# Optimization experiments

Measured on AMD Instinct MI355X. Metric: run time of the kernel, lower is better.

Reference implementation:

```python
import jax, jax.numpy as jnp
import numpy as np

DIM = 96
HEADS = 6
WIN = (4, 4, 4)
SHIFT = (2, 2, 2)
MLP_HIDDEN = 384
GRID = (16, 64, 64)
B = 2
EPS = 1e-5


def _rel_idx():
    # relative position index [N, N] into the (2w-1)^3 bias table
    c = np.stack(np.meshgrid(*[np.arange(w) for w in WIN], indexing='ij')).reshape(3, -1)
    rel = c[:, :, None] - c[:, None, :]
    for d, w in enumerate(WIN):
        rel[d] += w - 1
    rel[0] *= (2 * WIN[1] - 1) * (2 * WIN[2] - 1)
    rel[1] *= 2 * WIN[2] - 1
    return jnp.asarray(rel.sum(0))

REL_IDX = _rel_idx()  # [64, 64]


def _layernorm(x, g, b):
    m = jnp.mean(x, axis=-1, keepdims=True)
    v = jnp.mean(jnp.square(x - m), axis=-1, keepdims=True)
    return (x - m) * jax.lax.rsqrt(v + EPS) * g + b


def setup_inputs() -> dict:
    key = jax.random.key(0)
    ks = jax.random.split(key, 8)
    nI, nX, nT = GRID
    L = nI * nX * nT
    std = 0.02
    return {
        'x': jax.random.normal(ks[0], (B, L, DIM), dtype=jnp.float32),
        'norm1_g': jnp.ones((DIM,), jnp.float32),
        'norm1_b': jnp.zeros((DIM,), jnp.float32),
        'qkv_w': jax.random.normal(ks[1], (DIM, 3 * DIM), jnp.float32) * std,
        'qkv_b': jnp.zeros((3 * DIM,), jnp.float32),
        'proj_w': jax.random.normal(ks[2], (DIM, DIM), jnp.float32) * std,
        'proj_b': jnp.zeros((DIM,), jnp.float32),
        'bias_table': jax.random.normal(ks[3], ((2 * WIN[0] - 1) * (2 * WIN[1] - 1) * (2 * WIN[2] - 1), HEADS), jnp.float32) * std,
        'norm2_g': jnp.ones((DIM,), jnp.float32),
        'norm2_b': jnp.zeros((DIM,), jnp.float32),
        'mlp_w1': jax.random.normal(ks[4], (DIM, MLP_HIDDEN), jnp.float32) * std,
        'mlp_b1': jnp.zeros((MLP_HIDDEN,), jnp.float32),
        'mlp_w2': jax.random.normal(ks[5], (MLP_HIDDEN, DIM), jnp.float32) * std,
        'mlp_b2': jnp.zeros((DIM,), jnp.float32),
        'nI': nI, 'nX': nX, 'nT': nT,
    }


def reference(x, norm1_g, norm1_b, qkv_w, qkv_b, proj_w, proj_b, bias_table,
              norm2_g, norm2_b, mlp_w1, mlp_b1, mlp_w2, mlp_b2, nI, nX, nT):
    Bb, L, C = x.shape
    wI, wX, wT = WIN
    sI, sX, sT = SHIFT
    N = wI * wX * wT
    hd = C // HEADS

    h = _layernorm(x, norm1_g, norm1_b).reshape(Bb, nI, nX, nT, C)
    h = jnp.roll(h, (-sI, -sX, -sT), axis=(1, 2, 3))
    # window partition -> [B*nW, N, C]
    h = h.reshape(Bb, nI // wI, wI, nX // wX, wX, nT // wT, wT, C)
    h = h.transpose(0, 1, 3, 5, 2, 4, 6, 7).reshape(-1, N, C)
    B_ = h.shape[0]

    qkv = (h @ qkv_w + qkv_b).reshape(B_, N, 3, HEADS, hd).transpose(2, 0, 3, 1, 4)
    q, k, v = qkv[0], qkv[1], qkv[2]  # each [B_, H, N, hd]
    attn = jnp.einsum('bhnd,bhmd->bhnm', q, k) * (hd ** -0.5)
    bias = bias_table[REL_IDX].transpose(2, 0, 1)  # [H, N, N]
    attn = jax.nn.softmax(attn + bias, axis=-1)
    o = jnp.einsum('bhnm,bhmd->bhnd', attn, v).transpose(0, 2, 1, 3).reshape(B_, N, C)
    o = o @ proj_w + proj_b

    # window reverse -> [B, nI, nX, nT, C]
    o = o.reshape(Bb, nI // wI, nX // wX, nT // wT, wI, wX, wT, C)
    o = o.transpose(0, 1, 4, 2, 5, 3, 6, 7).reshape(Bb, nI, nX, nT, C)
    o = jnp.roll(o, (sI, sX, sT), axis=(1, 2, 3)).reshape(Bb, L, C)

    x = x + o
    h2 = _layernorm(x, norm2_g, norm2_b)
    x = x + (jax.nn.gelu(h2 @ mlp_w1 + mlp_b1, approximate=False) @ mlp_w2 + mlp_b2)
    return x
```

## Files before the change

### kernel.cpp

```cpp
#include <hip/hip_runtime.h>
#include <math.h>


typedef __attribute__((ext_vector_type(8))) short short8;
typedef __attribute__((ext_vector_type(4))) float floatx4;
typedef unsigned short ushort;
typedef unsigned int uint;

__device__ __forceinline__ ushort f2bf(float f) {
    union { float f; uint u; } v; v.f = f;
    uint r = v.u + 0x7FFFu + ((v.u >> 16) & 1u);
    return (ushort)(r >> 16);
}
__device__ __forceinline__ uint pk2(float a, float b) {
    return (uint)f2bf(a) | ((uint)f2bf(b) << 16);
}
union U8 { uint u[4]; short8 s8; };

#define WS_QKV  0
#define WS_PROJ (288 * 104)
#define WS_W1   (384 * 104)
#define WS_W2   (768 * 104)

__global__ __launch_bounds__(512, 8)
void convert_w(const float* __restrict__ qkvw, const float* __restrict__ projw,
               const float* __restrict__ w1, const float* __restrict__ w2,
               ushort* __restrict__ ws)
{
    const int idx = blockIdx.x * 512 + threadIdx.x;
    const int kk = idx / 1152;
    const int r  = idx - kk * 1152;
    const int k0 = 2 * kk, k1 = k0 + 1;
    float a, b;
    if (r < 288)      { a = qkvw[k0 * 288 + r];              b = qkvw[k1 * 288 + r]; }
    else if (r < 384) { const int c = r - 288;  a = projw[k0 * 96 + c];  b = projw[k1 * 96 + c]; }
    else if (r < 768) { const int c = r - 384;  a = w1[k0 * 384 + c];    b = w1[k1 * 384 + c]; }
    else {
        const int c0 = r - 768;
        const int jt = c0 / 96, c = c0 - jt * 96;
        a = w2[(jt * 96 + k0) * 96 + c];
        b = w2[(jt * 96 + k1) * 96 + c];
    }
    *(uint*)&ws[r * 104 + k0] = pk2(a, b);
}

__global__ __launch_bounds__(512, 4)
void swin_attn_kernel(const float* __restrict__ x,
                      const float* __restrict__ n1g, const float* __restrict__ n1b,
                      const ushort* __restrict__ ws,
                      const float* __restrict__ qkvb,
                      const float* __restrict__ projb,
                      const float* __restrict__ btab,
                      float* __restrict__ y)
{
    __shared__ __align__(16) ushort hA[64 * 104];
    __shared__ __align__(16) ushort qS[6 * 64 * 20];
    __shared__ __align__(16) ushort kS[6 * 64 * 20];
    __shared__ __align__(16) ushort vT[6 * 16 * 68];
    __shared__ __align__(16) ushort oA[64 * 104];
    __shared__ __align__(16) float  bias_s[343 * 6];

    const int tid = threadIdx.x;
    const int wid = blockIdx.x;
    const int bb = wid >> 10;
    const int wi = (wid >> 8) & 3;
    const int wx = (wid >> 4) & 15;
    const int wt = wid & 15;

    for (int i = tid; i < 343 * 6; i += 512) bias_s[i] = btab[i];
    {
        const int n = tid >> 3, p = tid & 7;
        const int a = n >> 4, c = (n >> 2) & 3, e = n & 3;
        const int gi = (wi * 4 + a + 2) & 15;
        const int gx = (wx * 4 + c + 2) & 63;
        const int gt = (wt * 4 + e + 2) & 63;
        const int l = (gi << 12) + (gx << 6) + gt;
        const float* src = x + ((size_t)bb * 65536 + l) * 96 + p * 12;
        float v[12];
        #pragma unroll
        for (int i = 0; i < 3; ++i) {
            const float4 t = *(const float4*)(src + i * 4);
            v[i*4+0] = t.x; v[i*4+1] = t.y; v[i*4+2] = t.z; v[i*4+3] = t.w;
        }
        float s = 0.f, ss = 0.f;
        #pragma unroll
        for (int i = 0; i < 12; ++i) { s += v[i]; ss += v[i] * v[i]; }
        s  += __shfl_xor(s, 1);  s  += __shfl_xor(s, 2);  s  += __shfl_xor(s, 4);
        ss += __shfl_xor(ss, 1); ss += __shfl_xor(ss, 2); ss += __shfl_xor(ss, 4);
        const float mean = s * (1.f / 96.f);
        const float rstd = rsqrtf(ss * (1.f / 96.f) - mean * mean + 1e-5f);
        float nv[12];
        #pragma unroll
        for (int i = 0; i < 12; ++i) {
            const int ch = p * 12 + i;
            nv[i] = (v[i] - mean) * rstd * n1g[ch] + n1b[ch];
        }
        #pragma unroll
        for (int j = 0; j < 6; ++j)
            *(uint*)&hA[n * 104 + p * 12 + 2 * j] = pk2(nv[2*j], nv[2*j+1]);
    }
    __syncthreads();

    const int wv = tid >> 6, lane = tid & 63;
    const int lr = lane & 15, lg = lane >> 4;
    const int tr = wv >> 1;
    const int chf = wv & 1;

    const short8 hfr0 = *(const short8*)&hA[(tr*16 + lr) * 104 +  0 + lg * 8];
    const short8 hfr1 = *(const short8*)&hA[(tr*16 + lr) * 104 + 32 + lg * 8];
    const short8 hfr2 = *(const short8*)&hA[(tr*16 + lr) * 104 + 64 + lg * 8];

    #pragma unroll
    for (int jt = 0; jt < 3; ++jt) {
#define QKV_CT(CT) { \
        const ushort* wp = ws + WS_QKV + ((jt*96 + chf*48 + (CT)*16 + lr) * 104 + lg * 8); \
        floatx4 acc = {0.f,0.f,0.f,0.f}; \
        acc = __builtin_amdgcn_mfma_f32_16x16x32_bf16(*(const short8*)(wp     ), hfr0, acc, 0,0,0); \
        acc = __builtin_amdgcn_mfma_f32_16x16x32_bf16(*(const short8*)(wp + 32), hfr1, acc, 0,0,0); \
        acc = __builtin_amdgcn_mfma_f32_16x16x32_bf16(*(const short8*)(wp + 64), hfr2, acc, 0,0,0); \
        const int colb = chf*48 + (CT)*16 + lg*4; \
        const int hh = colb >> 4, db = colb & 15; \
        const int tok = tr*16 + lr; \
        const float4 b4 = *(const float4*)&qkvb[jt*96 + colb]; \
        const float v0 = acc[0] + b4.x, v1 = acc[1] + b4.y; \
        const float v2 = acc[2] + b4.z, v3 = acc[3] + b4.w; \
        if (jt == 0) { \
            *(uint*)&qS[(hh*64 + tok)*20 + db    ] = pk2(v0*0.25f, v1*0.25f); \
            *(uint*)&qS[(hh*64 + tok)*20 + db + 2] = pk2(v2*0.25f, v3*0.25f); \
        } else if (jt == 1) { \
            *(uint*)&kS[(hh*64 + tok)*20 + db    ] = pk2(v0, v1); \
            *(uint*)&kS[(hh*64 + tok)*20 + db + 2] = pk2(v2, v3); \
        } else { \
            vT[(hh*16 + db + 0)*68 + tok] = f2bf(v0); \
            vT[(hh*16 + db + 1)*68 + tok] = f2bf(v1); \
            vT[(hh*16 + db + 2)*68 + tok] = f2bf(v2); \
            vT[(hh*16 + db + 3)*68 + tok] = f2bf(v3); \
        } }
        QKV_CT(0) QKV_CT(1) QKV_CT(2)
#undef QKV_CT
    }
    __syncthreads();

    {
        const int c1 = lr >> 2, e1 = lr & 3;
        #pragma unroll
        for (int iu = 0; iu < 3; ++iu) {
            const int unit = wv * 3 + iu;
            const int head = unit >> 2, qt = unit & 3;
            U8 qf;
            { const uint2 qb = *(const uint2*)&qS[(head*64 + qt*16 + lr)*20 + lg*4];
              qf.u[0] = qb.x; qf.u[1] = qb.y; qf.u[2] = 0u; qf.u[3] = 0u; }
            float sc[16];
            #pragma unroll
            for (int kt = 0; kt < 4; ++kt) {
                U8 kf;
                { const uint2 kb = *(const uint2*)&kS[(head*64 + kt*16 + lr)*20 + lg*4];
                  kf.u[0] = kb.x; kf.u[1] = kb.y; kf.u[2] = 0u; kf.u[3] = 0u; }
                floatx4 z = {0.f,0.f,0.f,0.f};
                z = __builtin_amdgcn_mfma_f32_16x16x32_bf16(kf.s8, qf.s8, z, 0,0,0);
                #pragma unroll
                for (int r = 0; r < 4; ++r) {
                    const int ridx = ((qt - kt + 3)*7 + (c1 - lg + 3))*7 + (e1 - r + 3);
                    sc[kt*4+r] = z[r] + bias_s[ridx*6 + head];
                }
            }
            float mx = sc[0];
            #pragma unroll
            for (int j = 1; j < 16; ++j) mx = fmaxf(mx, sc[j]);
            float pn[16]; float sum = 0.f;
            #pragma unroll
            for (int j = 0; j < 16; ++j) { pn[j] = __expf(sc[j] - mx); sum += pn[j]; }
            const float inv = 1.f / sum;
            #pragma unroll
            for (int j = 0; j < 16; ++j) pn[j] *= inv;
            U8 pf0, pf1;
            pf0.u[0] = pk2(pn[0],  pn[1]);  pf0.u[1] = pk2(pn[2],  pn[3]);
            pf0.u[2] = pk2(pn[4],  pn[5]);  pf0.u[3] = pk2(pn[6],  pn[7]);
            pf1.u[0] = pk2(pn[8],  pn[9]);  pf1.u[1] = pk2(pn[10], pn[11]);
            pf1.u[2] = pk2(pn[12], pn[13]); pf1.u[3] = pk2(pn[14], pn[15]);
            U8 vf0, vf1;
            { const uint2 va = *(const uint2*)&vT[(head*16 + lr)*68 +  0 + lg*4];
              const uint2 vb = *(const uint2*)&vT[(head*16 + lr)*68 + 16 + lg*4];
              vf0.u[0] = va.x; vf0.u[1] = va.y; vf0.u[2] = vb.x; vf0.u[3] = vb.y; }
            { const uint2 va = *(const uint2*)&vT[(head*16 + lr)*68 + 32 + lg*4];
              const uint2 vb = *(const uint2*)&vT[(head*16 + lr)*68 + 48 + lg*4];
              vf1.u[0] = va.x; vf1.u[1] = va.y; vf1.u[2] = vb.x; vf1.u[3] = vb.y; }
            floatx4 o = {0.f,0.f,0.f,0.f};
            o = __builtin_amdgcn_mfma_f32_16x16x32_bf16(vf0.s8, pf0.s8, o, 0,0,0);
            o = __builtin_amdgcn_mfma_f32_16x16x32_bf16(vf1.s8, pf1.s8, o, 0,0,0);
            *(uint*)&oA[(qt*16 + lr)*104 + head*16 + lg*4    ] = pk2(o[0], o[1]);
            *(uint*)&oA[(qt*16 + lr)*104 + head*16 + lg*4 + 2] = pk2(o[2], o[3]);
        }
    }
    __syncthreads();

    {
        const short8 ofr0 = *(const short8*)&oA[(tr*16 + lr) * 104 +  0 + lg * 8];
        const short8 ofr1 = *(const short8*)&oA[(tr*16 + lr) * 104 + 32 + lg * 8];
        const short8 ofr2 = *(const short8*)&oA[(tr*16 + lr) * 104 + 64 + lg * 8];
        const int n = tr*16 + lr;
        const int gi = (wi * 4 + tr + 2) & 15;
        const int gx = (wx * 4 + (lr >> 2) + 2) & 63;
        const int gt = (wt * 4 + (lr & 3) + 2) & 63;
        const int l = (gi << 12) + (gx << 6) + gt;
        const size_t tbase = ((size_t)bb * 65536 + l) * 96;
        (void)n;
#define PRJ_CT(CT) { \
        const ushort* wp = ws + WS_PROJ + ((chf*48 + (CT)*16 + lr) * 104 + lg * 8); \
        floatx4 acc = {0.f,0.f,0.f,0.f}; \
        acc = __builtin_amdgcn_mfma_f32_16x16x32_bf16(*(const short8*)(wp     ), ofr0, acc, 0,0,0); \
        acc = __builtin_amdgcn_mfma_f32_16x16x32_bf16(*(const short8*)(wp + 32), ofr1, acc, 0,0,0); \
        acc = __builtin_amdgcn_mfma_f32_16x16x32_bf16(*(const short8*)(wp + 64), ofr2, acc, 0,0,0); \
        const int colb = chf*48 + (CT)*16 + lg*4; \
        const float4 pb4 = *(const float4*)&projb[colb]; \
        const float4 xv = *(const float4*)(x + tbase + colb); \
        float4 r; \
        r.x = xv.x + acc[0] + pb4.x; \
        r.y = xv.y + acc[1] + pb4.y; \
        r.z = xv.z + acc[2] + pb4.z; \
        r.w = xv.w + acc[3] + pb4.w; \
        *(float4*)(y + tbase + colb) = r; }
        PRJ_CT(0) PRJ_CT(1) PRJ_CT(2)
#undef PRJ_CT
    }
}

__global__ __launch_bounds__(512, 4)
void swin_mlp_kernel(const float* __restrict__ y,
                     const float* __restrict__ n2g, const float* __restrict__ n2b,
                     const ushort* __restrict__ ws,
                     const float* __restrict__ b1p, const float* __restrict__ b2p,
                     float* __restrict__ out)
{
    __shared__ __align__(16) ushort h2A[128 * 104];
    __shared__ __align__(16) ushort t1A[128 * 104];

    const int tid = threadIdx.x;
    const size_t tok0 = (size_t)blockIdx.x * 128;

    {
        const int tk = tid >> 2, q4 = tid & 3;
        const float* src = y + (tok0 + tk) * 96 + q4 * 24;
        float v[24];
        #pragma unroll
        for (int i = 0; i < 6; ++i) {
            const float4 t = *(const float4*)(src + i * 4);
            v[i*4+0]=t.x; v[i*4+1]=t.y; v[i*4+2]=t.z; v[i*4+3]=t.w;
        }
        float s = 0.f, ss = 0.f;
        #pragma unroll
        for (int i = 0; i < 24; ++i) { s += v[i]; ss += v[i]*v[i]; }
        s += __shfl_xor(s, 1); s += __shfl_xor(s, 2);
        ss += __shfl_xor(ss, 1); ss += __shfl_xor(ss, 2);
        const float mean = s * (1.f/96.f);
        const float rstd = rsqrtf(ss * (1.f/96.f) - mean*mean + 1e-5f);
        float nv[24];
        #pragma unroll
        for (int i = 0; i < 24; ++i) {
            const int ch = q4 * 24 + i;
            nv[i] = (v[i]-mean)*rstd*n2g[ch] + n2b[ch];
        }
        #pragma unroll
        for (int j = 0; j < 12; ++j)
            *(uint*)&h2A[tk * 104 + q4 * 24 + 2 * j] = pk2(nv[2*j], nv[2*j+1]);
    }
    __syncthreads();

    const int wv = tid >> 6, lane = tid & 63;
    const int lr = lane & 15, lg = lane >> 4;
    const int trow = (wv*16 + lr) * 104;

    const short8 hfr0 = *(const short8*)&h2A[trow +  0 + lg * 8];
    const short8 hfr1 = *(const short8*)&h2A[trow + 32 + lg * 8];
    const short8 hfr2 = *(const short8*)&h2A[trow + 64 + lg * 8];

    floatx4 a0 = {0.f,0.f,0.f,0.f}, a1 = {0.f,0.f,0.f,0.f}, a2 = {0.f,0.f,0.f,0.f},
            a3 = {0.f,0.f,0.f,0.f}, a4 = {0.f,0.f,0.f,0.f}, a5 = {0.f,0.f,0.f,0.f};

    #pragma unroll
    for (int jt = 0; jt < 4; ++jt) {
#define M1_CT(CT) { \
        const ushort* wp = ws + WS_W1 + ((jt*96 + (CT)*16 + lr) * 104 + lg * 8); \
        floatx4 g = {0.f,0.f,0.f,0.f}; \
        g = __builtin_amdgcn_mfma_f32_16x16x32_bf16(*(const short8*)(wp     ), hfr0, g, 0,0,0); \
        g = __builtin_amdgcn_mfma_f32_16x16x32_bf16(*(const short8*)(wp + 32), hfr1, g, 0,0,0); \
        g = __builtin_amdgcn_mfma_f32_16x16x32_bf16(*(const short8*)(wp + 64), hfr2, g, 0,0,0); \
        const float4 bv = *(const float4*)&b1p[jt*96 + (CT)*16 + lg*4]; \
        float t0 = g[0] + bv.x, t1 = g[1] + bv.y, t2 = g[2] + bv.z, t3 = g[3] + bv.w; \
        t0 = 0.5f * t0 * (1.f + erff(t0 * 0.70710678118654752f)); \
        t1 = 0.5f * t1 * (1.f + erff(t1 * 0.70710678118654752f)); \
        t2 = 0.5f * t2 * (1.f + erff(t2 * 0.70710678118654752f)); \
        t3 = 0.5f * t3 * (1.f + erff(t3 * 0.70710678118654752f)); \
        *(uint*)&t1A[trow + (CT)*16 + lg*4    ] = pk2(t0, t1); \
        *(uint*)&t1A[trow + (CT)*16 + lg*4 + 2] = pk2(t2, t3); }
        M1_CT(0) M1_CT(1) M1_CT(2) M1_CT(3) M1_CT(4) M1_CT(5)
#undef M1_CT
        asm volatile("" ::: "memory");
        const short8 tf0 = *(const short8*)&t1A[trow +  0 + lg * 8];
        const short8 tf1 = *(const short8*)&t1A[trow + 32 + lg * 8];
        const short8 tf2 = *(const short8*)&t1A[trow + 64 + lg * 8];
#define M2_CO(CO, AO) { \
        const ushort* wp = ws + WS_W2 + ((jt*96 + (CO)*16 + lr) * 104 + lg * 8); \
        AO = __builtin_amdgcn_mfma_f32_16x16x32_bf16(*(const short8*)(wp     ), tf0, AO, 0,0,0); \
        AO = __builtin_amdgcn_mfma_f32_16x16x32_bf16(*(const short8*)(wp + 32), tf1, AO, 0,0,0); \
        AO = __builtin_amdgcn_mfma_f32_16x16x32_bf16(*(const short8*)(wp + 64), tf2, AO, 0,0,0); }
        M2_CO(0, a0) M2_CO(1, a1) M2_CO(2, a2) M2_CO(3, a3) M2_CO(4, a4) M2_CO(5, a5)
#undef M2_CO
        asm volatile("" ::: "memory");
    }

    {
        const size_t base = (tok0 + wv*16 + lr) * 96;
#define M_OUT(CO, AO) { \
        const int colb = (CO)*16 + lg*4; \
        const float4 b2v = *(const float4*)&b2p[colb]; \
        const float4 yv = *(const float4*)(y + base + colb); \
        float4 r; \
        r.x = yv.x + AO[0] + b2v.x; \
        r.y = yv.y + AO[1] + b2v.y; \
        r.z = yv.z + AO[2] + b2v.z; \
        r.w = yv.w + AO[3] + b2v.w; \
        *(float4*)(out + base + colb) = r; }
        M_OUT(0, a0) M_OUT(1, a1) M_OUT(2, a2) M_OUT(3, a3) M_OUT(4, a4) M_OUT(5, a5)
#undef M_OUT
    }
}

extern "C" void kernel_launch(void* const* d_in, const int* in_sizes, int n_in,
                              void* d_out, int out_size, void* d_ws, size_t ws_size,
                              hipStream_t stream) {
    (void)in_sizes; (void)n_in; (void)ws_size; (void)out_size;
    const float* x     = (const float*)d_in[0];
    const float* n1g   = (const float*)d_in[1];
    const float* n1b   = (const float*)d_in[2];
    const float* qkvw  = (const float*)d_in[3];
    const float* qkvb  = (const float*)d_in[4];
    const float* projw = (const float*)d_in[5];
    const float* projb = (const float*)d_in[6];
    const float* btab  = (const float*)d_in[7];
    const float* n2g   = (const float*)d_in[8];
    const float* n2b   = (const float*)d_in[9];
    const float* w1    = (const float*)d_in[10];
    const float* b1    = (const float*)d_in[11];
    const float* w2    = (const float*)d_in[12];
    const float* b2    = (const float*)d_in[13];
    float* out = (float*)d_out;
    ushort* ws = (ushort*)d_ws;

    convert_w<<<108, 512, 0, stream>>>(qkvw, projw, w1, w2, ws);
    swin_attn_kernel<<<2048, 512, 0, stream>>>(x, n1g, n1b, ws, qkvb, projb, btab, out);
    swin_mlp_kernel<<<1024, 512, 0, stream>>>(out, n2g, n2b, ws, b1, b2, out);
}
```

Before: 276.8 us.

## Alias LDS buffers, keep Q in registers, use tanh GELU, raise occupancy

The attention kernel keeps the Q fragments in registers instead of staging them through shared memory, and re-partitions heads so each wave reuses its own token tile. The input and output LDS tiles are aliased into one buffer. The MLP kernel aliases its hidden-activation tile onto the normed-input tile, adding a barrier before reuse. Launch bounds are raised to allow more resident blocks, and the exact erf GELU is replaced by the tanh approximation, which is cheaper but numerically differs from the reference's exact GELU.

```diff
diff --git a/kernel.cpp b/kernel.cpp
--- a/kernel.cpp
+++ b/kernel.cpp
@@ -14,6 +14,12 @@
 }
 __device__ __forceinline__ uint pk2(float a, float b) {
     return (uint)f2bf(a) | ((uint)f2bf(b) << 16);
+}
+__device__ __forceinline__ float gelu_f(float x) {
+    const float s = 0.7978845608028654f * fmaf(0.044715f * x, x * x, x);
+    const float e = __expf(2.f * s);
+    const float th = 1.f - 2.f / (e + 1.f);
+    return 0.5f * x * (1.f + th);
 }
 union U8 { uint u[4]; short8 s8; };
 
@@ -44,7 +50,7 @@
     *(uint*)&ws[r * 104 + k0] = pk2(a, b);
 }
 
-__global__ __launch_bounds__(512, 4)
+__global__ __launch_bounds__(512, 6)
 void swin_attn_kernel(const float* __restrict__ x,
                       const float* __restrict__ n1g, const float* __restrict__ n1b,
                       const ushort* __restrict__ ws,
@@ -53,12 +59,12 @@
                       const float* __restrict__ btab,
                       float* __restrict__ y)
 {
-    __shared__ __align__(16) ushort hA[64 * 104];
-    __shared__ __align__(16) ushort qS[6 * 64 * 20];
+    __shared__ __align__(16) ushort hoA[64 * 104];
     __shared__ __align__(16) ushort kS[6 * 64 * 20];
     __shared__ __align__(16) ushort vT[6 * 16 * 68];
-    __shared__ __align__(16) ushort oA[64 * 104];
     __shared__ __align__(16) float  bias_s[343 * 6];
+    ushort* hA = hoA;
+    ushort* oA = hoA;
 
     const int tid = threadIdx.x;
     const int wid = blockIdx.x;
@@ -110,6 +116,7 @@
     const short8 hfr1 = *(const short8*)&hA[(tr*16 + lr) * 104 + 32 + lg * 8];
     const short8 hfr2 = *(const short8*)&hA[(tr*16 + lr) * 104 + 64 + lg * 8];
 
+    uint qp[3][2];
     #pragma unroll
     for (int jt = 0; jt < 3; ++jt) {
 #define QKV_CT(CT) { \
@@ -125,8 +132,8 @@
         const float v0 = acc[0] + b4.x, v1 = acc[1] + b4.y; \
         const float v2 = acc[2] + b4.z, v3 = acc[3] + b4.w; \
         if (jt == 0) { \
-            *(uint*)&qS[(hh*64 + tok)*20 + db    ] = pk2(v0*0.25f, v1*0.25f); \
-            *(uint*)&qS[(hh*64 + tok)*20 + db + 2] = pk2(v2*0.25f, v3*0.25f); \
+            qp[CT][0] = pk2(v0*0.25f, v1*0.25f); \
+            qp[CT][1] = pk2(v2*0.25f, v3*0.25f); \
         } else if (jt == 1) { \
             *(uint*)&kS[(hh*64 + tok)*20 + db    ] = pk2(v0, v1); \
             *(uint*)&kS[(hh*64 + tok)*20 + db + 2] = pk2(v2, v3); \
@@ -145,11 +152,9 @@
         const int c1 = lr >> 2, e1 = lr & 3;
         #pragma unroll
         for (int iu = 0; iu < 3; ++iu) {
-            const int unit = wv * 3 + iu;
-            const int head = unit >> 2, qt = unit & 3;
+            const int head = 3 * chf + iu;
             U8 qf;
-            { const uint2 qb = *(const uint2*)&qS[(head*64 + qt*16 + lr)*20 + lg*4];
-              qf.u[0] = qb.x; qf.u[1] = qb.y; qf.u[2] = 0u; qf.u[3] = 0u; }
+            qf.u[0] = qp[iu][0]; qf.u[1] = qp[iu][1]; qf.u[2] = 0u; qf.u[3] = 0u;
             float sc[16];
             #pragma unroll
             for (int kt = 0; kt < 4; ++kt) {
@@ -160,7 +165,7 @@
                 z = __builtin_amdgcn_mfma_f32_16x16x32_bf16(kf.s8, qf.s8, z, 0,0,0);
                 #pragma unroll
                 for (int r = 0; r < 4; ++r) {
-                    const int ridx = ((qt - kt + 3)*7 + (c1 - lg + 3))*7 + (e1 - r + 3);
+                    const int ridx = ((tr - kt + 3)*7 + (c1 - lg + 3))*7 + (e1 - r + 3);
                     sc[kt*4+r] = z[r] + bias_s[ridx*6 + head];
                 }
             }
@@ -188,8 +193,8 @@
             floatx4 o = {0.f,0.f,0.f,0.f};
             o = __builtin_amdgcn_mfma_f32_16x16x32_bf16(vf0.s8, pf0.s8, o, 0,0,0);
             o = __builtin_amdgcn_mfma_f32_16x16x32_bf16(vf1.s8, pf1.s8, o, 0,0,0);
-            *(uint*)&oA[(qt*16 + lr)*104 + head*16 + lg*4    ] = pk2(o[0], o[1]);
-            *(uint*)&oA[(qt*16 + lr)*104 + head*16 + lg*4 + 2] = pk2(o[2], o[3]);
+            *(uint*)&oA[(tr*16 + lr)*104 + head*16 + lg*4    ] = pk2(o[0], o[1]);
+            *(uint*)&oA[(tr*16 + lr)*104 + head*16 + lg*4 + 2] = pk2(o[2], o[3]);
         }
     }
     __syncthreads();
@@ -198,13 +203,11 @@
         const short8 ofr0 = *(const short8*)&oA[(tr*16 + lr) * 104 +  0 + lg * 8];
         const short8 ofr1 = *(const short8*)&oA[(tr*16 + lr) * 104 + 32 + lg * 8];
         const short8 ofr2 = *(const short8*)&oA[(tr*16 + lr) * 104 + 64 + lg * 8];
-        const int n = tr*16 + lr;
         const int gi = (wi * 4 + tr + 2) & 15;
         const int gx = (wx * 4 + (lr >> 2) + 2) & 63;
         const int gt = (wt * 4 + (lr & 3) + 2) & 63;
         const int l = (gi << 12) + (gx << 6) + gt;
         const size_t tbase = ((size_t)bb * 65536 + l) * 96;
-        (void)n;
 #define PRJ_CT(CT) { \
         const ushort* wp = ws + WS_PROJ + ((chf*48 + (CT)*16 + lr) * 104 + lg * 8); \
         floatx4 acc = {0.f,0.f,0.f,0.f}; \
@@ -225,7 +228,7 @@
     }
 }
 
-__global__ __launch_bounds__(512, 4)
+__global__ __launch_bounds__(512, 8)
 void swin_mlp_kernel(const float* __restrict__ y,
                      const float* __restrict__ n2g, const float* __restrict__ n2b,
                      const ushort* __restrict__ ws,
@@ -233,7 +236,7 @@
                      float* __restrict__ out)
 {
     __shared__ __align__(16) ushort h2A[128 * 104];
-    __shared__ __align__(16) ushort t1A[128 * 104];
+    ushort* t1A = h2A;
 
     const int tid = threadIdx.x;
     const size_t tok0 = (size_t)blockIdx.x * 128;
@@ -273,6 +276,7 @@
     const short8 hfr0 = *(const short8*)&h2A[trow +  0 + lg * 8];
     const short8 hfr1 = *(const short8*)&h2A[trow + 32 + lg * 8];
     const short8 hfr2 = *(const short8*)&h2A[trow + 64 + lg * 8];
+    __syncthreads();
 
     floatx4 a0 = {0.f,0.f,0.f,0.f}, a1 = {0.f,0.f,0.f,0.f}, a2 = {0.f,0.f,0.f,0.f},
             a3 = {0.f,0.f,0.f,0.f}, a4 = {0.f,0.f,0.f,0.f}, a5 = {0.f,0.f,0.f,0.f};
@@ -286,11 +290,10 @@
         g = __builtin_amdgcn_mfma_f32_16x16x32_bf16(*(const short8*)(wp + 32), hfr1, g, 0,0,0); \
         g = __builtin_amdgcn_mfma_f32_16x16x32_bf16(*(const short8*)(wp + 64), hfr2, g, 0,0,0); \
         const float4 bv = *(const float4*)&b1p[jt*96 + (CT)*16 + lg*4]; \
-        float t0 = g[0] + bv.x, t1 = g[1] + bv.y, t2 = g[2] + bv.z, t3 = g[3] + bv.w; \
-        t0 = 0.5f * t0 * (1.f + erff(t0 * 0.70710678118654752f)); \
-        t1 = 0.5f * t1 * (1.f + erff(t1 * 0.70710678118654752f)); \
-        t2 = 0.5f * t2 * (1.f + erff(t2 * 0.70710678118654752f)); \
-        t3 = 0.5f * t3 * (1.f + erff(t3 * 0.70710678118654752f)); \
+        const float t0 = gelu_f(g[0] + bv.x); \
+        const float t1 = gelu_f(g[1] + bv.y); \
+        const float t2 = gelu_f(g[2] + bv.z); \
+        const float t3 = gelu_f(g[3] + bv.w); \
         *(uint*)&t1A[trow + (CT)*16 + lg*4    ] = pk2(t0, t1); \
         *(uint*)&t1A[trow + (CT)*16 + lg*4 + 2] = pk2(t2, t3); }
         M1_CT(0) M1_CT(1) M1_CT(2) M1_CT(3) M1_CT(4) M1_CT(5)
```

Result: slower. 334.8 us (+20.9%).
